# Kernel tuning notes

Hardware: AMD Instinct MI355X
Metric: run time of the kernel (lower is better)

## Reference

```python
import jax, jax.numpy as jnp
import numpy as np

B, S, E, H = 2, 2048, 1024, 16
DH = E // H
SCALE = DH ** -0.5

def setup_inputs() -> dict:
    key = jax.random.key(0)
    ks = jax.random.split(key, 5)
    w_std = (2.0 / (E + E)) ** 0.5  # xavier-ish scale
    return {
        'x': jax.random.normal(ks[0], (B, S, E), jnp.float32),
        'Wq': jax.random.normal(ks[1], (E, E), jnp.float32) * w_std,
        'bq': jnp.zeros((E,), jnp.float32),
        'Wk': jax.random.normal(ks[2], (E, E), jnp.float32) * w_std,
        'bk': jnp.zeros((E,), jnp.float32),
        'Wv': jax.random.normal(ks[3], (E, E), jnp.float32) * w_std,
        'bv': jnp.zeros((E,), jnp.float32),
        'Wo': jax.random.normal(ks[4], (E, E), jnp.float32) * w_std,
        'bo': jnp.zeros((E,), jnp.float32),
    }

def reference(x, Wq, bq, Wk, bk, Wv, bv, Wo, bo):
    # self-attention: query = key = value = x; torch Linear: y = x @ W.T + b
    q = (x @ Wq.T + bq) * SCALE            # [B,S,E]
    k = x @ Wk.T + bk
    v = x @ Wv.T + bv
    # split heads -> [B,S,H,DH]
    q = q.reshape(B, S, H, DH)
    k = k.reshape(B, S, H, DH)
    v = v.reshape(B, S, H, DH)
    # explicit attention matrix [B,H,S,S] (faithful to unfused bmm path)
    scores = jnp.einsum('bqhd,bkhd->bhqk', q, k)
    probs = jax.nn.softmax(scores, axis=-1)
    attn = jnp.einsum('bhqk,bkhd->bqhd', probs, v).reshape(B, S, E)
    return attn @ Wo.T + bo                # [B,S,E]
```

## Files before the change

kernel.cpp:

```cpp
#include <hip/hip_runtime.h>
#include <stdint.h>

#define BB 2
#define SS 2048
#define EE 1024
#define HH 16
#define DHD 64
#define MM (BB*SS)
#define QSCALE (0.125f * 1.4426950408889634f)

typedef __bf16 bf16;
typedef __bf16 bf16x8 __attribute__((ext_vector_type(8)));
typedef __bf16 bf16x4 __attribute__((ext_vector_type(4)));
typedef float  f32x4  __attribute__((ext_vector_type(4)));
typedef unsigned short ushort8 __attribute__((ext_vector_type(8)));

#define MFMA16(a,b,c) __builtin_amdgcn_mfma_f32_16x16x32_bf16(a,b,c,0,0,0)

__device__ __forceinline__ void gload_lds16(const void* g, void* l) {
  __builtin_amdgcn_global_load_lds(
      (const __attribute__((address_space(1))) unsigned int*)g,
      (__attribute__((address_space(3))) unsigned int*)l, 16, 0, 0);
}

__device__ __forceinline__ unsigned short f2bf(float f) {
  union { float f; unsigned u; } v; v.f = f;
  return (unsigned short)((v.u + 0x7FFFu + ((v.u >> 16) & 1u)) >> 16);
}

__global__ void convert_kernel(const float* __restrict__ x,
                               const float* __restrict__ wq, const float* __restrict__ wk,
                               const float* __restrict__ wv, const float* __restrict__ wo,
                               unsigned short* __restrict__ xbf,
                               unsigned short* __restrict__ wqb, unsigned short* __restrict__ wkb,
                               unsigned short* __restrict__ wvb, unsigned short* __restrict__ wob) {
  long t = (long)blockIdx.x * blockDim.x + threadIdx.x;
  long base = t * 8;
  const float* src; unsigned short* dst; long off;
  if (base < 4194304L) { src = x; dst = xbf; off = base; }
  else {
    long r = base - 4194304L; int j = (int)(r >> 20); off = r & 1048575L;
    src = (j==0)?wq:(j==1)?wk:(j==2)?wv:wo;
    dst = (j==0)?wqb:(j==1)?wkb:(j==2)?wvb:wob;
  }
  const float4* s4 = (const float4*)(src + off);
  float4 a = s4[0], b = s4[1];
  ushort8 o;
  o[0]=f2bf(a.x); o[1]=f2bf(a.y); o[2]=f2bf(a.z); o[3]=f2bf(a.w);
  o[4]=f2bf(b.x); o[5]=f2bf(b.y); o[6]=f2bf(b.z); o[7]=f2bf(b.w);
  *(ushort8*)(dst + off) = o;
}

__global__ __launch_bounds__(256) void qkv_gemm(
    const bf16* __restrict__ xbf,
    const bf16* __restrict__ wqb, const bf16* __restrict__ wkb, const bf16* __restrict__ wvb,
    const float* __restrict__ bq, const float* __restrict__ bk, const float* __restrict__ bv,
    bf16* __restrict__ Q, bf16* __restrict__ K, bf16* __restrict__ VT) {
  __shared__ char As[128*64] __attribute__((aligned(16)));
  __shared__ char Bs[128*64] __attribute__((aligned(16)));
  const int tid = threadIdx.x;
  const int bm = blockIdx.y * 128;
  const int bnG = blockIdx.x * 128;
  const int proj = bnG >> 10;
  const int bn = bnG & 1023;
  const bf16* wsel = (proj==0)?wqb:(proj==1)?wkb:wvb;
  const float* bias = (proj==0)?bq:(proj==1)?bk:bv;

  const int lane = tid & 63, w = tid >> 6;
  const int wm = (w>>1)*64, wn = (w&1)*64;
  const int c = lane & 15, g = lane >> 4;

  const int sr = tid >> 2;
  const int scb = ((tid & 3) * 16) ^ ((sr & 3) << 4);
  const char* a0 = (const char*)xbf  + ((size_t)(bm + sr     ) * 1024) * 2 + scb;
  const char* a1 = (const char*)xbf  + ((size_t)(bm + 64 + sr) * 1024) * 2 + scb;
  const char* b0 = (const char*)wsel + ((size_t)(bn + sr     ) * 1024) * 2 + scb;
  const char* b1 = (const char*)wsel + ((size_t)(bn + 64 + sr) * 1024) * 2 + scb;
  char* lA0 = As + tid*16; char* lA1 = As + 4096 + tid*16;
  char* lB0 = Bs + tid*16; char* lB1 = Bs + 4096 + tid*16;

  int aoff[4], boff[4];
#pragma unroll
  for (int mt=0; mt<4; ++mt) { int rr = wm + mt*16 + c; aoff[mt] = rr*64 + ((g*16) ^ ((rr&3)<<4)); }
#pragma unroll
  for (int nt=0; nt<4; ++nt) { int rr = wn + nt*16 + c; boff[nt] = rr*64 + ((g*16) ^ ((rr&3)<<4)); }

  f32x4 acc[4][4];
#pragma unroll
  for (int mt=0; mt<4; ++mt)
#pragma unroll
    for (int nt=0; nt<4; ++nt) acc[mt][nt] = (f32x4){0.f,0.f,0.f,0.f};

  for (int kt = 0; kt < 32; ++kt) {
    const size_t kb = (size_t)kt * 64;
    gload_lds16(a0 + kb, lA0); gload_lds16(a1 + kb, lA1);
    gload_lds16(b0 + kb, lB0); gload_lds16(b1 + kb, lB1);
    __syncthreads();
    bf16x8 af[4], bfv[4];
#pragma unroll
    for (int mt=0; mt<4; ++mt) af[mt] = *(const bf16x8*)(As + aoff[mt]);
#pragma unroll
    for (int nt=0; nt<4; ++nt) bfv[nt] = *(const bf16x8*)(Bs + boff[nt]);
#pragma unroll
    for (int mt=0; mt<4; ++mt)
#pragma unroll
      for (int nt=0; nt<4; ++nt)
        acc[mt][nt] = MFMA16(af[mt], bfv[nt], acc[mt][nt]);
    __syncthreads();
  }

  const int bidx = bm >> 11;
  const int srow = bm & 2047;
#pragma unroll
  for (int nt=0; nt<4; ++nt) {
    const int n = bn + wn + nt*16 + c;
    const float bv_ = bias[n];
    const int h = n >> 6, d = n & 63;
#pragma unroll
    for (int mt=0; mt<4; ++mt) {
      f32x4 a = acc[mt][nt];
      const int m0 = wm + mt*16 + g*4;
      if (proj == 0) {
#pragma unroll
        for (int r=0;r<4;++r) {
          int s = srow + m0 + r;
          Q[(((size_t)(bidx*16 + h))*2048 + s)*64 + d] = (bf16)((a[r] + bv_) * QSCALE);
        }
      } else if (proj == 1) {
#pragma unroll
        for (int r=0;r<4;++r) {
          int s = srow + m0 + r;
          K[(((size_t)(bidx*16 + h))*2048 + s)*64 + d] = (bf16)(a[r] + bv_);
        }
      } else {
        bf16x4 pk;
#pragma unroll
        for (int r=0;r<4;++r) pk[r] = (bf16)(a[r] + bv_);
        *(bf16x4*)(VT + (((size_t)(bidx*16 + h))*64 + d)*2048 + (srow + m0)) = pk;
      }
    }
  }
}

__global__ __launch_bounds__(256) void attn_kernel(
    const bf16* __restrict__ Q, const bf16* __restrict__ K,
    const bf16* __restrict__ VT, bf16* __restrict__ attn_out) {
  __shared__ char lds[32768] __attribute__((aligned(16)));
  const int tid = threadIdx.x;
  const int lane = tid & 63, w = tid >> 6;
  const int c = lane & 15, g = lane >> 4;
  const int x7 = c & 7;
  const int bh = blockIdx.y;
  const int qb = blockIdx.x * 64 + w * 16;
  const bf16* Qh = Q + (size_t)bh * 2048 * 64;
  const char* Khb = (const char*)(K  + (size_t)bh * 2048 * 64);
  const char* Vhb = (const char*)(VT + (size_t)bh * 64 * 2048);

  const int srow = tid >> 3, schunk = tid & 7;
  const int ssw = ((schunk ^ (srow & 7)) << 4);
  const char* srcK = Khb + (size_t)srow * 128  + ssw;
  const char* srcV = Vhb + (size_t)srow * 4096 + ssw;

#define ATT_STAGE(buf, kv) { \
    const char* sk_ = srcK + (size_t)(kv) * 128; \
    const char* sv_ = srcV + (size_t)(kv) * 2; \
    char* d_ = lds + (buf) * 16384 + tid * 16; \
    gload_lds16(sk_,            d_); \
    gload_lds16(sk_ + 32*128,   d_ + 4096); \
    gload_lds16(sv_,            d_ + 8192); \
    gload_lds16(sv_ + 32*4096,  d_ + 12288); \
  }

  bf16x8 qf0 = *(const bf16x8*)(Qh + (size_t)(qb + c)*64 + g*8);
  bf16x8 qf1 = *(const bf16x8*)(Qh + (size_t)(qb + c)*64 + 32 + g*8);

  f32x4 o[4];
#pragma unroll
  for (int dt=0; dt<4; ++dt) o[dt] = (f32x4){0.f,0.f,0.f,0.f};
  float m = -1e30f, l = 0.f;

  ATT_STAGE(0, 0);
  for (int t = 0; t < 32; ++t) {
    const int cur = t & 1;
    if (t < 31) {
      ATT_STAGE(cur ^ 1, (t + 1) * 64);
      asm volatile("s_waitcnt vmcnt(4)" ::: "memory");
    } else {
      asm volatile("s_waitcnt vmcnt(0)" ::: "memory");
    }
    __builtin_amdgcn_s_barrier();

    const char* Kl = lds + cur * 16384;
    const char* Vl = Kl + 8192;

    f32x4 st[4];
#pragma unroll
    for (int ks = 0; ks < 4; ++ks) {
      const char* kr = Kl + (ks*16 + c) * 128;
      bf16x8 k0 = *(const bf16x8*)(kr + (((g    ) ^ x7) << 4));
      bf16x8 k1 = *(const bf16x8*)(kr + (((g + 4) ^ x7) << 4));
      f32x4 z = (f32x4){0.f,0.f,0.f,0.f};
      z = MFMA16(k0, qf0, z);
      z = MFMA16(k1, qf1, z);
      st[ks] = z;
    }

    float tmax = -1e30f;
#pragma unroll
    for (int ks = 0; ks < 4; ++ks)
      tmax = fmaxf(tmax, fmaxf(fmaxf(st[ks][0], st[ks][1]), fmaxf(st[ks][2], st[ks][3])));
    tmax = fmaxf(tmax, __shfl_xor(tmax, 16, 64));
    tmax = fmaxf(tmax, __shfl_xor(tmax, 32, 64));
    const float mnew = fmaxf(m, tmax);
    const float corr = __builtin_exp2f(m - mnew);
    float p[4][4]; float ps = 0.f;
#pragma unroll
    for (int ks = 0; ks < 4; ++ks)
#pragma unroll
      for (int r = 0; r < 4; ++r) { p[ks][r] = __builtin_exp2f(st[ks][r] - mnew); ps += p[ks][r]; }
    ps += __shfl_xor(ps, 16, 64);
    ps += __shfl_xor(ps, 32, 64);
    l = l * corr + ps;
    m = mnew;
#pragma unroll
    for (int dt=0; dt<4; ++dt) o[dt] *= corr;

    bf16x8 pfA, pfB;
#pragma unroll
    for (int r = 0; r < 4; ++r) {
      pfA[r] = (bf16)p[0][r]; pfA[4+r] = (bf16)p[1][r];
      pfB[r] = (bf16)p[2][r]; pfB[4+r] = (bf16)p[3][r];
    }

#pragma unroll
    for (int dt = 0; dt < 4; ++dt) {
      const char* vr = Vl + (dt*16 + c) * 128;
      const int i8 = (g & 1) * 8, gh = g >> 1;
      bf16x4 a0 = *(const bf16x4*)(vr + (((gh    ) ^ x7) << 4) + i8);
      bf16x4 a1 = *(const bf16x4*)(vr + (((gh + 2) ^ x7) << 4) + i8);
      bf16x4 b0 = *(const bf16x4*)(vr + (((gh + 4) ^ x7) << 4) + i8);
      bf16x4 b1 = *(const bf16x4*)(vr + (((gh + 6) ^ x7) << 4) + i8);
      bf16x8 vfA = __builtin_shufflevector(a0, a1, 0,1,2,3,4,5,6,7);
      bf16x8 vfB = __builtin_shufflevector(b0, b1, 0,1,2,3,4,5,6,7);
      o[dt] = MFMA16(vfA, pfA, o[dt]);
      o[dt] = MFMA16(vfB, pfB, o[dt]);
    }

    asm volatile("s_waitcnt lgkmcnt(0)" ::: "memory");
    __builtin_amdgcn_s_barrier();
  }
#undef ATT_STAGE

  const float inv = 1.0f / l;
  const int srow_q = qb + c;
  const int b = bh >> 4, h = bh & 15;
  bf16* outrow = attn_out + ((size_t)(b*2048 + srow_q))*1024 + h*64;
#pragma unroll
  for (int dt=0; dt<4; ++dt) {
    bf16x4 ov;
#pragma unroll
    for (int r=0;r<4;++r) ov[r] = (bf16)(o[dt][r] * inv);
    *(bf16x4*)(outrow + dt*16 + g*4) = ov;
  }
}

__global__ __launch_bounds__(256) void out_gemm(
    const bf16* __restrict__ A, const bf16* __restrict__ W,
    const float* __restrict__ bias, float* __restrict__ out) {
  __shared__ char As[128*64] __attribute__((aligned(16)));
  __shared__ char Bs[128*64] __attribute__((aligned(16)));
  const int tid = threadIdx.x;
  const int bm = blockIdx.y * 128, bn = blockIdx.x * 128;
  const int lane = tid & 63, w = tid >> 6;
  const int wm = (w>>1)*64, wn = (w&1)*64;
  const int c = lane & 15, g = lane >> 4;

  const int sr = tid >> 2;
  const int scb = ((tid & 3) * 16) ^ ((sr & 3) << 4);
  const char* a0 = (const char*)A + ((size_t)(bm + sr     ) * 1024) * 2 + scb;
  const char* a1 = (const char*)A + ((size_t)(bm + 64 + sr) * 1024) * 2 + scb;
  const char* b0 = (const char*)W + ((size_t)(bn + sr     ) * 1024) * 2 + scb;
  const char* b1 = (const char*)W + ((size_t)(bn + 64 + sr) * 1024) * 2 + scb;
  char* lA0 = As + tid*16; char* lA1 = As + 4096 + tid*16;
  char* lB0 = Bs + tid*16; char* lB1 = Bs + 4096 + tid*16;

  int aoff[4], boff[4];
#pragma unroll
  for (int mt=0; mt<4; ++mt) { int rr = wm + mt*16 + c; aoff[mt] = rr*64 + ((g*16) ^ ((rr&3)<<4)); }
#pragma unroll
  for (int nt=0; nt<4; ++nt) { int rr = wn + nt*16 + c; boff[nt] = rr*64 + ((g*16) ^ ((rr&3)<<4)); }

  f32x4 acc[4][4];
#pragma unroll
  for (int mt=0; mt<4; ++mt)
#pragma unroll
    for (int nt=0; nt<4; ++nt) acc[mt][nt] = (f32x4){0.f,0.f,0.f,0.f};

  for (int kt = 0; kt < 32; ++kt) {
    const size_t kb = (size_t)kt * 64;
    gload_lds16(a0 + kb, lA0); gload_lds16(a1 + kb, lA1);
    gload_lds16(b0 + kb, lB0); gload_lds16(b1 + kb, lB1);
    __syncthreads();
    bf16x8 af[4], bfv[4];
#pragma unroll
    for (int mt=0; mt<4; ++mt) af[mt] = *(const bf16x8*)(As + aoff[mt]);
#pragma unroll
    for (int nt=0; nt<4; ++nt) bfv[nt] = *(const bf16x8*)(Bs + boff[nt]);
#pragma unroll
    for (int mt=0; mt<4; ++mt)
#pragma unroll
      for (int nt=0; nt<4; ++nt)
        acc[mt][nt] = MFMA16(af[mt], bfv[nt], acc[mt][nt]);
    __syncthreads();
  }

#pragma unroll
  for (int nt=0; nt<4; ++nt) {
    const int n = bn + wn + nt*16 + c;
    const float bv_ = bias[n];
#pragma unroll
    for (int mt=0; mt<4; ++mt) {
      const int m0 = bm + wm + mt*16 + g*4;
#pragma unroll
      for (int r=0;r<4;++r) out[(size_t)(m0 + r)*1024 + n] = acc[mt][nt][r] + bv_;
    }
  }
}

extern "C" void kernel_launch(void* const* d_in, const int* in_sizes, int n_in,
                              void* d_out, int out_size, void* d_ws, size_t ws_size,
                              hipStream_t stream) {
  const float* x  = (const float*)d_in[0];
  const float* Wq = (const float*)d_in[1];
  const float* bq = (const float*)d_in[2];
  const float* Wk = (const float*)d_in[3];
  const float* bk = (const float*)d_in[4];
  const float* Wv = (const float*)d_in[5];
  const float* bv = (const float*)d_in[6];
  const float* Wo = (const float*)d_in[7];
  const float* bo = (const float*)d_in[8];

  char* ws = (char*)d_ws;
  const size_t MiB = 1u << 20;
  unsigned short* xbf = (unsigned short*)(ws);
  unsigned short* wqb = (unsigned short*)(ws +  8*MiB);
  unsigned short* wkb = (unsigned short*)(ws + 10*MiB);
  unsigned short* wvb = (unsigned short*)(ws + 12*MiB);
  unsigned short* wob = (unsigned short*)(ws + 14*MiB);
  bf16* Qb    = (bf16*)(ws + 16*MiB);
  bf16* Kb    = (bf16*)(ws + 24*MiB);
  bf16* VTb   = (bf16*)(ws + 32*MiB);
  bf16* attnb = (bf16*)(ws + 40*MiB);

  convert_kernel<<<4096, 256, 0, stream>>>(x, Wq, Wk, Wv, Wo, xbf, wqb, wkb, wvb, wob);
  qkv_gemm<<<dim3(24, 32), 256, 0, stream>>>(
      (const bf16*)xbf, (const bf16*)wqb, (const bf16*)wkb, (const bf16*)wvb,
      bq, bk, bv, Qb, Kb, VTb);
  attn_kernel<<<dim3(32, 32), 256, 0, stream>>>(Qb, Kb, VTb, attnb);
  out_gemm<<<dim3(8, 32), 256, 0, stream>>>(attnb, (const bf16*)wob, bo, (float*)d_out);
}
```

Measured before the change: 230.3 us.

## Double-buffer GEMM LDS loads and add lazy softmax rescale in attention

Both projection GEMMs move from a single LDS buffer with two __syncthreads per k-step to a double-buffered pipeline that prefetches the next k-tile with global_load_lds and waits through explicit vmcnt and barrier. The attention kernel skips the running-max update and the rescale of the output accumulator whenever every lane's new tile max stays within a bound of the current max. It also raises wave priority around the MFMA sections and rebalances the max reduction tree. The aim is to hide global load latency in the GEMMs and cut exp and rescale work in the softmax, at the cost of twice the LDS per GEMM block and a wave-uniform branch.

```diff
diff --git a/kernel.cpp b/kernel.cpp
--- a/kernel.cpp
+++ b/kernel.cpp
@@ -51,13 +51,21 @@
   *(ushort8*)(dst + off) = o;
 }
 
+#define G_STAGE(kbuf, kt) { \
+    const size_t kb_ = (size_t)(kt) * 64; \
+    char* d_ = lds + (kbuf) * 16384 + tid * 16; \
+    gload_lds16(a0 + kb_, d_); \
+    gload_lds16(a1 + kb_, d_ + 4096); \
+    gload_lds16(b0 + kb_, d_ + 8192); \
+    gload_lds16(b1 + kb_, d_ + 12288); \
+  }
+
 __global__ __launch_bounds__(256) void qkv_gemm(
     const bf16* __restrict__ xbf,
     const bf16* __restrict__ wqb, const bf16* __restrict__ wkb, const bf16* __restrict__ wvb,
     const float* __restrict__ bq, const float* __restrict__ bk, const float* __restrict__ bv,
     bf16* __restrict__ Q, bf16* __restrict__ K, bf16* __restrict__ VT) {
-  __shared__ char As[128*64] __attribute__((aligned(16)));
-  __shared__ char Bs[128*64] __attribute__((aligned(16)));
+  __shared__ char lds[32768] __attribute__((aligned(16)));
   const int tid = threadIdx.x;
   const int bm = blockIdx.y * 128;
   const int bnG = blockIdx.x * 128;
@@ -76,14 +84,12 @@
   const char* a1 = (const char*)xbf  + ((size_t)(bm + 64 + sr) * 1024) * 2 + scb;
   const char* b0 = (const char*)wsel + ((size_t)(bn + sr     ) * 1024) * 2 + scb;
   const char* b1 = (const char*)wsel + ((size_t)(bn + 64 + sr) * 1024) * 2 + scb;
-  char* lA0 = As + tid*16; char* lA1 = As + 4096 + tid*16;
-  char* lB0 = Bs + tid*16; char* lB1 = Bs + 4096 + tid*16;
 
   int aoff[4], boff[4];
 #pragma unroll
   for (int mt=0; mt<4; ++mt) { int rr = wm + mt*16 + c; aoff[mt] = rr*64 + ((g*16) ^ ((rr&3)<<4)); }
 #pragma unroll
-  for (int nt=0; nt<4; ++nt) { int rr = wn + nt*16 + c; boff[nt] = rr*64 + ((g*16) ^ ((rr&3)<<4)); }
+  for (int nt=0; nt<4; ++nt) { int rr = wn + nt*16 + c; boff[nt] = 8192 + rr*64 + ((g*16) ^ ((rr&3)<<4)); }
 
   f32x4 acc[4][4];
 #pragma unroll
@@ -91,22 +97,29 @@
 #pragma unroll
     for (int nt=0; nt<4; ++nt) acc[mt][nt] = (f32x4){0.f,0.f,0.f,0.f};
 
+  G_STAGE(0, 0);
   for (int kt = 0; kt < 32; ++kt) {
-    const size_t kb = (size_t)kt * 64;
-    gload_lds16(a0 + kb, lA0); gload_lds16(a1 + kb, lA1);
-    gload_lds16(b0 + kb, lB0); gload_lds16(b1 + kb, lB1);
-    __syncthreads();
+    const int cur = kt & 1;
+    if (kt < 31) {
+      G_STAGE(cur ^ 1, kt + 1);
+      asm volatile("s_waitcnt vmcnt(4)" ::: "memory");
+    } else {
+      asm volatile("s_waitcnt vmcnt(0)" ::: "memory");
+    }
+    __builtin_amdgcn_s_barrier();
+    const char* Ts = lds + cur * 16384;
     bf16x8 af[4], bfv[4];
 #pragma unroll
-    for (int mt=0; mt<4; ++mt) af[mt] = *(const bf16x8*)(As + aoff[mt]);
-#pragma unroll
-    for (int nt=0; nt<4; ++nt) bfv[nt] = *(const bf16x8*)(Bs + boff[nt]);
+    for (int mt=0; mt<4; ++mt) af[mt] = *(const bf16x8*)(Ts + aoff[mt]);
+#pragma unroll
+    for (int nt=0; nt<4; ++nt) bfv[nt] = *(const bf16x8*)(Ts + boff[nt]);
 #pragma unroll
     for (int mt=0; mt<4; ++mt)
 #pragma unroll
       for (int nt=0; nt<4; ++nt)
         acc[mt][nt] = MFMA16(af[mt], bfv[nt], acc[mt][nt]);
-    __syncthreads();
+    asm volatile("s_waitcnt lgkmcnt(0)" ::: "memory");
+    __builtin_amdgcn_s_barrier();
   }
 
   const int bidx = bm >> 11;
@@ -145,7 +158,7 @@
 __global__ __launch_bounds__(256) void attn_kernel(
     const bf16* __restrict__ Q, const bf16* __restrict__ K,
     const bf16* __restrict__ VT, bf16* __restrict__ attn_out) {
-  __shared__ char lds[32768] __attribute__((aligned(16)));
+  __shared__ char alds[32768] __attribute__((aligned(16)));
   const int tid = threadIdx.x;
   const int lane = tid & 63, w = tid >> 6;
   const int c = lane & 15, g = lane >> 4;
@@ -164,7 +177,7 @@
 #define ATT_STAGE(buf, kv) { \
     const char* sk_ = srcK + (size_t)(kv) * 128; \
     const char* sv_ = srcV + (size_t)(kv) * 2; \
-    char* d_ = lds + (buf) * 16384 + tid * 16; \
+    char* d_ = alds + (buf) * 16384 + tid * 16; \
     gload_lds16(sk_,            d_); \
     gload_lds16(sk_ + 32*128,   d_ + 4096); \
     gload_lds16(sv_,            d_ + 8192); \
@@ -190,10 +203,11 @@
     }
     __builtin_amdgcn_s_barrier();
 
-    const char* Kl = lds + cur * 16384;
+    const char* Kl = alds + cur * 16384;
     const char* Vl = Kl + 8192;
 
     f32x4 st[4];
+    __builtin_amdgcn_s_setprio(1);
 #pragma unroll
     for (int ks = 0; ks < 4; ++ks) {
       const char* kr = Kl + (ks*16 + c) * 128;
@@ -204,26 +218,40 @@
       z = MFMA16(k1, qf1, z);
       st[ks] = z;
     }
-
-    float tmax = -1e30f;
-#pragma unroll
-    for (int ks = 0; ks < 4; ++ks)
-      tmax = fmaxf(tmax, fmaxf(fmaxf(st[ks][0], st[ks][1]), fmaxf(st[ks][2], st[ks][3])));
+    __builtin_amdgcn_s_setprio(0);
+
+    float m0_ = fmaxf(fmaxf(st[0][0], st[0][1]), st[0][2]);
+    float m1_ = fmaxf(fmaxf(st[0][3], st[1][0]), st[1][1]);
+    float m2_ = fmaxf(fmaxf(st[1][2], st[1][3]), st[2][0]);
+    float m3_ = fmaxf(fmaxf(st[2][1], st[2][2]), st[2][3]);
+    float m4_ = fmaxf(fmaxf(st[3][0], st[3][1]), st[3][2]);
+    float tmax = fmaxf(fmaxf(fmaxf(m0_, m1_), m2_), fmaxf(fmaxf(m3_, m4_), st[3][3]));
     tmax = fmaxf(tmax, __shfl_xor(tmax, 16, 64));
     tmax = fmaxf(tmax, __shfl_xor(tmax, 32, 64));
-    const float mnew = fmaxf(m, tmax);
-    const float corr = __builtin_exp2f(m - mnew);
+
     float p[4][4]; float ps = 0.f;
-#pragma unroll
-    for (int ks = 0; ks < 4; ++ks)
-#pragma unroll
-      for (int r = 0; r < 4; ++r) { p[ks][r] = __builtin_exp2f(st[ks][r] - mnew); ps += p[ks][r]; }
-    ps += __shfl_xor(ps, 16, 64);
-    ps += __shfl_xor(ps, 32, 64);
-    l = l * corr + ps;
-    m = mnew;
-#pragma unroll
-    for (int dt=0; dt<4; ++dt) o[dt] *= corr;
+    if (__all(tmax <= m + 8.f)) {
+#pragma unroll
+      for (int ks = 0; ks < 4; ++ks)
+#pragma unroll
+        for (int r = 0; r < 4; ++r) { p[ks][r] = __builtin_exp2f(st[ks][r] - m); ps += p[ks][r]; }
+      ps += __shfl_xor(ps, 16, 64);
+      ps += __shfl_xor(ps, 32, 64);
+      l += ps;
+    } else {
+      const float mnew = fmaxf(m, tmax);
+      const float corr = __builtin_exp2f(m - mnew);
+#pragma unroll
+      for (int ks = 0; ks < 4; ++ks)
+#pragma unroll
+        for (int r = 0; r < 4; ++r) { p[ks][r] = __builtin_exp2f(st[ks][r] - mnew); ps += p[ks][r]; }
+      ps += __shfl_xor(ps, 16, 64);
+      ps += __shfl_xor(ps, 32, 64);
+      l = l * corr + ps;
+      m = mnew;
+#pragma unroll
+      for (int dt=0; dt<4; ++dt) o[dt] *= corr;
+    }
 
     bf16x8 pfA, pfB;
 #pragma unroll
@@ -232,19 +260,21 @@
       pfB[r] = (bf16)p[2][r]; pfB[4+r] = (bf16)p[3][r];
     }
 
+    const int i8 = (g & 1) * 8, gh = g >> 1;
+    __builtin_amdgcn_s_setprio(1);
 #pragma unroll
     for (int dt = 0; dt < 4; ++dt) {
       const char* vr = Vl + (dt*16 + c) * 128;
-      const int i8 = (g & 1) * 8, gh = g >> 1;
-      bf16x4 a0 = *(const bf16x4*)(vr + (((gh    ) ^ x7) << 4) + i8);
-      bf16x4 a1 = *(const bf16x4*)(vr + (((gh + 2) ^ x7) << 4) + i8);
-      bf16x4 b0 = *(const bf16x4*)(vr + (((gh + 4) ^ x7) << 4) + i8);
-      bf16x4 b1 = *(const bf16x4*)(vr + (((gh + 6) ^ x7) << 4) + i8);
-      bf16x8 vfA = __builtin_shufflevector(a0, a1, 0,1,2,3,4,5,6,7);
-      bf16x8 vfB = __builtin_shufflevector(b0, b1, 0,1,2,3,4,5,6,7);
+      bf16x4 va0 = *(const bf16x4*)(vr + (((gh    ) ^ x7) << 4) + i8);
+      bf16x4 va1 = *(const bf16x4*)(vr + (((gh + 2) ^ x7) << 4) + i8);
+      bf16x4 vb0 = *(const bf16x4*)(vr + (((gh + 4) ^ x7) << 4) + i8);
+      bf16x4 vb1 = *(const bf16x4*)(vr + (((gh + 6) ^ x7) << 4) + i8);
+      bf16x8 vfA = __builtin_shufflevector(va0, va1, 0,1,2,3,4,5,6,7);
+      bf16x8 vfB = __builtin_shufflevector(vb0, vb1, 0,1,2,3,4,5,6,7);
       o[dt] = MFMA16(vfA, pfA, o[dt]);
       o[dt] = MFMA16(vfB, pfB, o[dt]);
     }
+    __builtin_amdgcn_s_setprio(0);
 
     asm volatile("s_waitcnt lgkmcnt(0)" ::: "memory");
     __builtin_amdgcn_s_barrier();
@@ -267,8 +297,7 @@
 __global__ __launch_bounds__(256) void out_gemm(
     const bf16* __restrict__ A, const bf16* __restrict__ W,
     const float* __restrict__ bias, float* __restrict__ out) {
-  __shared__ char As[128*64] __attribute__((aligned(16)));
-  __shared__ char Bs[128*64] __attribute__((aligned(16)));
+  __shared__ char lds[32768] __attribute__((aligned(16)));
   const int tid = threadIdx.x;
   const int bm = blockIdx.y * 128, bn = blockIdx.x * 128;
   const int lane = tid & 63, w = tid >> 6;
@@ -281,14 +310,12 @@
   const char* a1 = (const char*)A + ((size_t)(bm + 64 + sr) * 1024) * 2 + scb;
   const char* b0 = (const char*)W + ((size_t)(bn + sr     ) * 1024) * 2 + scb;
   const char* b1 = (const char*)W + ((size_t)(bn + 64 + sr) * 1024) * 2 + scb;
-  char* lA0 = As + tid*16; char* lA1 = As + 4096 + tid*16;
-  char* lB0 = Bs + tid*16; char* lB1 = Bs + 4096 + tid*16;
 
   int aoff[4], boff[4];
 #pragma unroll
   for (int mt=0; mt<4; ++mt) { int rr = wm + mt*16 + c; aoff[mt] = rr*64 + ((g*16) ^ ((rr&3)<<4)); }
 #pragma unroll
-  for (int nt=0; nt<4; ++nt) { int rr = wn + nt*16 + c; boff[nt] = rr*64 + ((g*16) ^ ((rr&3)<<4)); }
+  for (int nt=0; nt<4; ++nt) { int rr = wn + nt*16 + c; boff[nt] = 8192 + rr*64 + ((g*16) ^ ((rr&3)<<4)); }
 
   f32x4 acc[4][4];
 #pragma unroll
@@ -296,22 +323,29 @@
 #pragma unroll
     for (int nt=0; nt<4; ++nt) acc[mt][nt] = (f32x4){0.f,0.f,0.f,0.f};
 
+  G_STAGE(0, 0);
   for (int kt = 0; kt < 32; ++kt) {
-    const size_t kb = (size_t)kt * 64;
-    gload_lds16(a0 + kb, lA0); gload_lds16(a1 + kb, lA1);
-    gload_lds16(b0 + kb, lB0); gload_lds16(b1 + kb, lB1);
-    __syncthreads();
+    const int cur = kt & 1;
+    if (kt < 31) {
+      G_STAGE(cur ^ 1, kt + 1);
+      asm volatile("s_waitcnt vmcnt(4)" ::: "memory");
+    } else {
+      asm volatile("s_waitcnt vmcnt(0)" ::: "memory");
+    }
+    __builtin_amdgcn_s_barrier();
+    const char* Ts = lds + cur * 16384;
     bf16x8 af[4], bfv[4];
 #pragma unroll
-    for (int mt=0; mt<4; ++mt) af[mt] = *(const bf16x8*)(As + aoff[mt]);
-#pragma unroll
-    for (int nt=0; nt<4; ++nt) bfv[nt] = *(const bf16x8*)(Bs + boff[nt]);
+    for (int mt=0; mt<4; ++mt) af[mt] = *(const bf16x8*)(Ts + aoff[mt]);
+#pragma unroll
+    for (int nt=0; nt<4; ++nt) bfv[nt] = *(const bf16x8*)(Ts + boff[nt]);
 #pragma unroll
     for (int mt=0; mt<4; ++mt)
 #pragma unroll
       for (int nt=0; nt<4; ++nt)
         acc[mt][nt] = MFMA16(af[mt], bfv[nt], acc[mt][nt]);
-    __syncthreads();
+    asm volatile("s_waitcnt lgkmcnt(0)" ::: "memory");
+    __builtin_amdgcn_s_barrier();
   }
 
 #pragma unroll
```

Result: slower. 239.5 us (+4.0%).
